# Optimization experiments

Hardware: AMD Instinct MI355X
Metric: run time of the kernel (lower is better)

## Reference

```python
import jax, jax.numpy as jnp
import numpy as np

IMG_H, IMG_W = 256, 704
STRIDE = 4.0


def _make_cams(B, Ncam):
    K = np.array([[560.0, 0.0, 352.0], [0.0, 560.0, 128.0], [0.0, 0.0, 1.0]], dtype=np.float32)
    intrinsics = np.broadcast_to(K, (B, Ncam, 3, 3)).copy()
    c2e = np.zeros((Ncam, 4, 4), dtype=np.float32)
    for i in range(Ncam):
        th = 2.0 * np.pi * i / Ncam
        x_cam = np.array([np.sin(th), -np.cos(th), 0.0])   # camera right in ego
        y_cam = np.array([0.0, 0.0, -1.0])                  # camera down in ego
        z_cam = np.array([np.cos(th), np.sin(th), 0.0])     # camera forward in ego
        c2e[i, :3, 0] = x_cam
        c2e[i, :3, 1] = y_cam
        c2e[i, :3, 2] = z_cam
        c2e[i, :3, 3] = np.array([0.0, 0.0, 1.5])           # camera mounted 1.5m up
        c2e[i, 3, 3] = 1.0
    cam2ego = np.broadcast_to(c2e, (B, Ncam, 4, 4)).copy()
    return jnp.asarray(intrinsics), jnp.asarray(cam2ego)


def setup_inputs() -> dict:
    key = jax.random.key(0)
    B, Npts, Ncam = 4, 500000, 6
    Hf, Wf = 64, 176
    k1, k2, k3 = jax.random.split(key, 3)
    xy = jax.random.uniform(k1, (B, Npts, 2), minval=-50.0, maxval=50.0, dtype=jnp.float32)
    z = jax.random.uniform(k2, (B, Npts, 1), minval=-5.0, maxval=3.0, dtype=jnp.float32)
    inten = jax.random.uniform(k3, (B, Npts, 1), dtype=jnp.float32)
    points_ego = jnp.concatenate([xy, z, inten], axis=-1)
    intrinsics, cam2ego = _make_cams(B, Ncam)
    # depth_values = linspace(1, 48, 48), step 1 -> edges [0.5, 1.5, ..., 48.5]
    dv = np.arange(48, dtype=np.float32) + 1.0
    step = 1.0
    edges = np.concatenate([[dv[0] - step / 2.0], dv + step / 2.0]).astype(np.float32)
    return {
        "points_ego": points_ego,
        "intrinsics": intrinsics,
        "cam2ego": cam2ego,
        "bin_edges": jnp.asarray(edges),
        "Hf": Hf,
        "Wf": Wf,
    }


def reference(points_ego, intrinsics, cam2ego, bin_edges, Hf, Wf):
    B, Npts, _ = points_ego.shape
    Ncam = intrinsics.shape[1]
    num_bins = bin_edges.shape[0] - 1

    ego2cam = jnp.linalg.inv(cam2ego)                       # (B,N,4,4)
    pts_h = jnp.concatenate([points_ego[..., :3], jnp.ones_like(points_ego[..., :1])], axis=-1)
    # project all points into all cameras at once: (B,N,P,4)
    p_cam = jnp.einsum('bnij,bpj->bnpi', ego2cam, pts_h)
    x, y, z = p_cam[..., 0], p_cam[..., 1], p_cam[..., 2]
    zc = jnp.maximum(z, 1e-6)

    fx = intrinsics[:, :, 0, 0][:, :, None]
    fy = intrinsics[:, :, 1, 1][:, :, None]
    cx = intrinsics[:, :, 0, 2][:, :, None]
    cy = intrinsics[:, :, 1, 2][:, :, None]
    u = fx * (x / zc) + cx
    v = fy * (y / zc) + cy

    valid = (z > 0.1) & (u >= 0) & (u <= IMG_W - 1) & (v >= 0) & (v <= IMG_H - 1)
    uf = jnp.floor(u / STRIDE).astype(jnp.int32)
    vf = jnp.floor(v / STRIDE).astype(jnp.int32)
    valid = valid & (uf >= 0) & (uf < Wf) & (vf >= 0) & (vf < Hf)
    uf = jnp.clip(uf, 0, Wf - 1)
    vf = jnp.clip(vf, 0, Hf - 1)

    pix = vf * Wf + uf                                      # (B,N,P)
    bn = (jnp.arange(B, dtype=jnp.int32)[:, None] * Ncam + jnp.arange(Ncam, dtype=jnp.int32)[None, :])
    seg = (bn[:, :, None] * (Hf * Wf) + pix).reshape(-1)    # global segment per (b, cam, pixel)

    # z-buffer: min depth per pixel (invalid points -> +inf, empty segments -> +inf)
    z_flat = jnp.where(valid, z, jnp.inf).reshape(-1)
    z_min = jax.ops.segment_min(z_flat, seg, num_segments=B * Ncam * Hf * Wf)

    d = jnp.clip(z_min, bin_edges[0] + 0.001, bin_edges[-1] - 0.001)
    # torch.bucketize(right=False): edges[i-1] < v <= edges[i]  ->  searchsorted side='left'
    bin_id = jnp.clip(jnp.searchsorted(bin_edges, d, side='left') - 1, 0, num_bins - 1)
    labels = jnp.where(jnp.isfinite(z_min), bin_id, -1).astype(jnp.int32)
    return labels.reshape(B, Ncam, Hf, Wf)
```

## Files before the change

kernel.cpp:

```cpp
#include <hip/hip_runtime.h>
#include <stdint.h>

#define BB    4
#define NCAM  6
#define HF    64
#define WF    176
#define IMGPIX (HF * WF)
#define NIMG  (BB * NCAM)
#define NPIX  (NIMG * IMGPIX)
#define NEDGE 49
#define SENTINEL 0x7F7F7F7F

#define GER_FMA     1
#define TRSM_RECIP  1
#define TRSM_FMA    1

__device__ void inv4_sgesv(const float* __restrict__ m,
                           const float* __restrict__ K,
                           float* __restrict__ out) {
#pragma clang fp contract(off)
    float a[4][4];
    for (int i = 0; i < 4; ++i)
        for (int j = 0; j < 4; ++j)
            a[i][j] = m[i * 4 + j];

    int ipiv[4];
    for (int j = 0; j < 4; ++j) {
        int p = j;
        float best = fabsf(a[j][j]);
        for (int i = j + 1; i < 4; ++i) {
            float v = fabsf(a[i][j]);
            if (v > best) { best = v; p = i; }
        }
        ipiv[j] = p;
        if (p != j) {
            for (int k = 0; k < 4; ++k) {
                float t = a[j][k]; a[j][k] = a[p][k]; a[p][k] = t;
            }
        }
        float r = 1.0f / a[j][j];
        for (int i = j + 1; i < 4; ++i) a[i][j] = a[i][j] * r;
        for (int k = j + 1; k < 4; ++k) {
            float temp = -a[j][k];
            for (int i = j + 1; i < 4; ++i) {
#if GER_FMA
                a[i][k] = __builtin_fmaf(a[i][j], temp, a[i][k]);
#else
                a[i][k] = a[i][k] + a[i][j] * temp;
#endif
            }
        }
    }

    float bmat[4][4];
    for (int i = 0; i < 4; ++i)
        for (int j = 0; j < 4; ++j)
            bmat[i][j] = (i == j) ? 1.0f : 0.0f;

    for (int k = 0; k < 4; ++k) {
        int p = ipiv[k];
        if (p != k) {
            for (int c = 0; c < 4; ++c) {
                float t = bmat[k][c]; bmat[k][c] = bmat[p][c]; bmat[p][c] = t;
            }
        }
    }

    for (int c = 0; c < 4; ++c) {
        for (int k = 0; k < 4; ++k) {
            float bk = bmat[k][c];
            for (int i = k + 1; i < 4; ++i) {
#if TRSM_FMA
                bmat[i][c] = __builtin_fmaf(a[i][k], -bk, bmat[i][c]);
#else
                bmat[i][c] = bmat[i][c] - a[i][k] * bk;
#endif
            }
        }
    }

#if TRSM_RECIP
    float rdiag[4];
    for (int k = 0; k < 4; ++k) rdiag[k] = 1.0f / a[k][k];
#endif
    for (int c = 0; c < 4; ++c) {
        for (int k = 3; k >= 0; --k) {
#if TRSM_RECIP
            bmat[k][c] = bmat[k][c] * rdiag[k];
#else
            bmat[k][c] = bmat[k][c] / a[k][k];
#endif
            float bk = bmat[k][c];
            for (int i = 0; i < k; ++i) {
#if TRSM_FMA
                bmat[i][c] = __builtin_fmaf(a[i][k], -bk, bmat[i][c]);
#else
                bmat[i][c] = bmat[i][c] - a[i][k] * bk;
#endif
            }
        }
    }

    for (int i = 0; i < 3; ++i)
        for (int j = 0; j < 4; ++j)
            out[i * 4 + j] = bmat[i][j];

    out[12] = K[0];
    out[13] = K[4];
    out[14] = K[2];
    out[15] = K[5];
}

__global__ void prep_cams_f32(const float* __restrict__ intr,
                              const float* __restrict__ c2e,
                              float* __restrict__ cams) {
    int idx = blockIdx.x * blockDim.x + threadIdx.x;
    if (idx >= NIMG) return;
    inv4_sgesv(c2e + idx * 16, intr + idx * 9, cams + idx * 16);
}

__device__ __forceinline__ bool project_pair(const float* M, float px, float py,
                                             float pz, float lo, float hi,
                                             int& pix, int& label) {
#pragma clang fp contract(off)
    float x = M[3];  x = x + M[2]  * pz;  x = x + M[1] * py;  x = x + M[0] * px;
    float y = M[7];  y = y + M[6]  * pz;  y = y + M[5] * py;  y = y + M[4] * px;
    float z = M[11]; z = z + M[10] * pz;  z = z + M[9] * py;  z = z + M[8] * px;

    float zc = fmaxf(z, 1e-6f);
    float u = M[12] * (x / zc) + M[14];
    float v = M[13] * (y / zc) + M[15];

    bool ok = (z > 0.1f) && (u >= 0.0f) && (u <= 703.0f) &&
              (v >= 0.0f) && (v <= 255.0f);

    int uf = (int)floorf(u / 4.0f);
    int vf = (int)floorf(v / 4.0f);
    pix = vf * WF + uf;

    float d = fminf(fmaxf(z, lo), hi);
    label = (int)ceilf(d - 0.5f) - 1;
    return ok;
}

__global__ __launch_bounds__(1024)
void scatter_lds(const float4* __restrict__ pts,
                 const float* __restrict__ cams,
                 const float* __restrict__ edges_f,
                 uint8_t* __restrict__ reps,
                 int npts, int csz) {
    __shared__ unsigned sbuf[IMGPIX];

    int g   = blockIdx.x;
    int img = blockIdx.y;
    int b   = img / NCAM;

    for (int i = threadIdx.x; i < IMGPIX; i += 1024)
        sbuf[i] = 0xFFFFFFFFu;
    __syncthreads();

    const float* M = cams + img * 16;
    float lo = edges_f[0]         + 0.001f;
    float hi = edges_f[NEDGE - 1] - 0.001f;

    int start = g * csz;
    int end   = start + csz; if (end > npts) end = npts;
    const float4* bp = pts + (size_t)b * npts;

    int p = start + (int)threadIdx.x;

    for (; p + 3 * 1024 < end; p += 4 * 1024) {
        float4 a0 = bp[p];
        float4 a1 = bp[p + 1024];
        float4 a2 = bp[p + 2048];
        float4 a3 = bp[p + 3072];

        int px0, l0, px1, l1, px2, l2, px3, l3;
        bool k0 = project_pair(M, a0.x, a0.y, a0.z, lo, hi, px0, l0);
        bool k1 = project_pair(M, a1.x, a1.y, a1.z, lo, hi, px1, l1);
        bool k2 = project_pair(M, a2.x, a2.y, a2.z, lo, hi, px2, l2);
        bool k3 = project_pair(M, a3.x, a3.y, a3.z, lo, hi, px3, l3);

        if (k0) atomicMin(&sbuf[px0], (unsigned)l0);
        if (k1) atomicMin(&sbuf[px1], (unsigned)l1);
        if (k2) atomicMin(&sbuf[px2], (unsigned)l2);
        if (k3) atomicMin(&sbuf[px3], (unsigned)l3);
    }
    for (; p < end; p += 1024) {
        float4 a0 = bp[p];
        int px0, l0;
        if (project_pair(M, a0.x, a0.y, a0.z, lo, hi, px0, l0))
            atomicMin(&sbuf[px0], (unsigned)l0);
    }
    __syncthreads();

    uint8_t* r = reps + (size_t)g * NPIX + (size_t)img * IMGPIX;
    for (int i = threadIdx.x; i < IMGPIX; i += 1024)
        r[i] = (uint8_t)sbuf[i];
}

__global__ void merge_reps(const uint8_t* __restrict__ reps, int G,
                           int* __restrict__ out) {
    int q = blockIdx.x * blockDim.x + threadIdx.x;
    if (q >= NPIX / 4) return;

    unsigned m = 0xFFFFFFFFu;
    for (int g = 0; g < G; ++g) {
        unsigned v = *(const unsigned*)(reps + (size_t)g * NPIX + q * 4);
        unsigned lo0 = (m & 0xFFu),        v0 = (v & 0xFFu);
        unsigned lo1 = (m >> 8) & 0xFFu,   v1 = (v >> 8) & 0xFFu;
        unsigned lo2 = (m >> 16) & 0xFFu,  v2 = (v >> 16) & 0xFFu;
        unsigned lo3 = (m >> 24),          v3 = (v >> 24);
        lo0 = v0 < lo0 ? v0 : lo0;
        lo1 = v1 < lo1 ? v1 : lo1;
        lo2 = v2 < lo2 ? v2 : lo2;
        lo3 = v3 < lo3 ? v3 : lo3;
        m = lo0 | (lo1 << 8) | (lo2 << 16) | (lo3 << 24);
    }
    int4 r;
    unsigned b0 = m & 0xFFu, b1 = (m >> 8) & 0xFFu,
             b2 = (m >> 16) & 0xFFu, b3 = m >> 24;
    r.x = (b0 == 255u) ? -1 : (int)b0;
    r.y = (b1 == 255u) ? -1 : (int)b1;
    r.z = (b2 == 255u) ? -1 : (int)b2;
    r.w = (b3 == 255u) ? -1 : (int)b3;
    ((int4*)out)[q] = r;
}

__global__ __launch_bounds__(256)
void scatter_minbin(const float4* __restrict__ pts,
                    const float* __restrict__ cams,
                    const float* __restrict__ edges_f,
                    int* __restrict__ out,
                    int npts) {
    int p = blockIdx.x * blockDim.x + threadIdx.x;
    int b = blockIdx.y;
    if (p >= npts) return;

    float4 pt = pts[(size_t)b * npts + p];
    float lo = edges_f[0]         + 0.001f;
    float hi = edges_f[NEDGE - 1] - 0.001f;

#pragma unroll
    for (int n = 0; n < NCAM; ++n) {
        const float* M = cams + (b * NCAM + n) * 16;
        int pix, label;
        if (project_pair(M, pt.x, pt.y, pt.z, lo, hi, pix, label)) {
            atomicMin(&out[(b * NCAM + n) * IMGPIX + pix], label);
        }
    }
}

__global__ void finalize(int* out) {
    int i = blockIdx.x * blockDim.x + threadIdx.x;
    if (i < NPIX && out[i] == SENTINEL) out[i] = -1;
}

extern "C" void kernel_launch(void* const* d_in, const int* in_sizes, int n_in,
                              void* d_out, int out_size, void* d_ws, size_t ws_size,
                              hipStream_t stream) {
    const float* points    = (const float*)d_in[0];
    const float* intrinsic = (const float*)d_in[1];
    const float* cam2ego   = (const float*)d_in[2];
    const float* edges     = (const float*)d_in[3];

    int npts = in_sizes[0] / (BB * 4);
    int* out = (int*)d_out;

    float*   cams = (float*)d_ws;
    uint8_t* reps = (uint8_t*)d_ws + 2048;

    int G = 0;
    if (ws_size > 2048 + (size_t)NPIX)
        G = (int)((ws_size - 2048) / (size_t)NPIX);
    if (G > 21) G = 21;

    prep_cams_f32<<<1, 64, 0, stream>>>(intrinsic, cam2ego, cams);

    if (G >= 1) {
        int csz = (npts + G - 1) / G;
        dim3 grid(G, NIMG);
        scatter_lds<<<grid, 1024, 0, stream>>>((const float4*)points, cams,
                                               edges, reps, npts, csz);
        merge_reps<<<(NPIX / 4 + 255) / 256, 256, 0, stream>>>(reps, G, out);
    } else {
        hipMemsetAsync(out, 0x7F, (size_t)NPIX * sizeof(int), stream);
        dim3 grid((npts + 255) / 256, BB);
        scatter_minbin<<<grid, 256, 0, stream>>>((const float4*)points, cams,
                                                 edges, out, npts);
        finalize<<<(NPIX + 255) / 256, 256, 0, stream>>>(out);
    }
}
```

Before: 48.83 us.

## Project each point into three cameras per block to reuse point loads

Each block now keeps three camera z-buffers in LDS (about 135 KB) and projects every loaded point into all three cameras, so point data is read from global memory once per three cameras instead of once per camera. The grid shrinks to 8 camera groups, and G rises to 30 to recover parallelism. The floor is replaced by a truncating cast on a multiply, which is only safe because negative u and v are already masked. The LDS init is vectorised and the output is packed into 32-bit stores. Occupancy drops to one block per CU because of the larger LDS footprint.

```diff
diff --git a/kernel.cpp b/kernel.cpp
--- a/kernel.cpp
+++ b/kernel.cpp
@@ -134,8 +134,8 @@
     bool ok = (z > 0.1f) && (u >= 0.0f) && (u <= 703.0f) &&
               (v >= 0.0f) && (v <= 255.0f);
 
-    int uf = (int)floorf(u / 4.0f);
-    int vf = (int)floorf(v / 4.0f);
+    int uf = (int)(u * 0.25f);
+    int vf = (int)(v * 0.25f);
     pix = vf * WF + uf;
 
     float d = fminf(fmaxf(z, lo), hi);
@@ -144,22 +144,26 @@
 }
 
 __global__ __launch_bounds__(1024)
-void scatter_lds(const float4* __restrict__ pts,
-                 const float* __restrict__ cams,
-                 const float* __restrict__ edges_f,
-                 uint8_t* __restrict__ reps,
-                 int npts, int csz) {
-    __shared__ unsigned sbuf[IMGPIX];
-
-    int g   = blockIdx.x;
-    int img = blockIdx.y;
-    int b   = img / NCAM;
-
-    for (int i = threadIdx.x; i < IMGPIX; i += 1024)
-        sbuf[i] = 0xFFFFFFFFu;
+void scatter_lds3(const float4* __restrict__ pts,
+                  const float* __restrict__ cams,
+                  const float* __restrict__ edges_f,
+                  uint8_t* __restrict__ reps,
+                  int npts, int csz) {
+    __shared__ unsigned sbuf[3 * IMGPIX];
+
+    int g    = blockIdx.x;
+    int grp  = blockIdx.y;
+    int img0 = grp * 3;
+    int b    = grp >> 1;
+
+    uint4* s4 = (uint4*)sbuf;
+    for (int i = threadIdx.x; i < 3 * IMGPIX / 4; i += 1024)
+        s4[i] = make_uint4(0xFFFFFFFFu, 0xFFFFFFFFu, 0xFFFFFFFFu, 0xFFFFFFFFu);
     __syncthreads();
 
-    const float* M = cams + img * 16;
+    const float* M0 = cams + (img0 + 0) * 16;
+    const float* M1 = cams + (img0 + 1) * 16;
+    const float* M2 = cams + (img0 + 2) * 16;
     float lo = edges_f[0]         + 0.001f;
     float hi = edges_f[NEDGE - 1] - 0.001f;
 
@@ -169,34 +173,49 @@
 
     int p = start + (int)threadIdx.x;
 
-    for (; p + 3 * 1024 < end; p += 4 * 1024) {
+    for (; p + 1024 < end; p += 2 * 1024) {
         float4 a0 = bp[p];
         float4 a1 = bp[p + 1024];
-        float4 a2 = bp[p + 2048];
-        float4 a3 = bp[p + 3072];
-
-        int px0, l0, px1, l1, px2, l2, px3, l3;
-        bool k0 = project_pair(M, a0.x, a0.y, a0.z, lo, hi, px0, l0);
-        bool k1 = project_pair(M, a1.x, a1.y, a1.z, lo, hi, px1, l1);
-        bool k2 = project_pair(M, a2.x, a2.y, a2.z, lo, hi, px2, l2);
-        bool k3 = project_pair(M, a3.x, a3.y, a3.z, lo, hi, px3, l3);
-
-        if (k0) atomicMin(&sbuf[px0], (unsigned)l0);
-        if (k1) atomicMin(&sbuf[px1], (unsigned)l1);
-        if (k2) atomicMin(&sbuf[px2], (unsigned)l2);
-        if (k3) atomicMin(&sbuf[px3], (unsigned)l3);
+
+        int x00, l00, x01, l01, x10, l10, x11, l11, x20, l20, x21, l21;
+        bool k00 = project_pair(M0, a0.x, a0.y, a0.z, lo, hi, x00, l00);
+        bool k01 = project_pair(M0, a1.x, a1.y, a1.z, lo, hi, x01, l01);
+        bool k10 = project_pair(M1, a0.x, a0.y, a0.z, lo, hi, x10, l10);
+        bool k11 = project_pair(M1, a1.x, a1.y, a1.z, lo, hi, x11, l11);
+        bool k20 = project_pair(M2, a0.x, a0.y, a0.z, lo, hi, x20, l20);
+        bool k21 = project_pair(M2, a1.x, a1.y, a1.z, lo, hi, x21, l21);
+
+        if (k00) atomicMin(&sbuf[x00],              (unsigned)l00);
+        if (k01) atomicMin(&sbuf[x01],              (unsigned)l01);
+        if (k10) atomicMin(&sbuf[IMGPIX + x10],     (unsigned)l10);
+        if (k11) atomicMin(&sbuf[IMGPIX + x11],     (unsigned)l11);
+        if (k20) atomicMin(&sbuf[2 * IMGPIX + x20], (unsigned)l20);
+        if (k21) atomicMin(&sbuf[2 * IMGPIX + x21], (unsigned)l21);
     }
     for (; p < end; p += 1024) {
         float4 a0 = bp[p];
-        int px0, l0;
-        if (project_pair(M, a0.x, a0.y, a0.z, lo, hi, px0, l0))
-            atomicMin(&sbuf[px0], (unsigned)l0);
+        int x0, l0, x1, l1, x2, l2;
+        if (project_pair(M0, a0.x, a0.y, a0.z, lo, hi, x0, l0))
+            atomicMin(&sbuf[x0], (unsigned)l0);
+        if (project_pair(M1, a0.x, a0.y, a0.z, lo, hi, x1, l1))
+            atomicMin(&sbuf[IMGPIX + x1], (unsigned)l1);
+        if (project_pair(M2, a0.x, a0.y, a0.z, lo, hi, x2, l2))
+            atomicMin(&sbuf[2 * IMGPIX + x2], (unsigned)l2);
     }
     __syncthreads();
 
-    uint8_t* r = reps + (size_t)g * NPIX + (size_t)img * IMGPIX;
-    for (int i = threadIdx.x; i < IMGPIX; i += 1024)
-        r[i] = (uint8_t)sbuf[i];
+    for (int c = 0; c < 3; ++c) {
+        unsigned* r32 = (unsigned*)(reps + (size_t)g * NPIX +
+                                    (size_t)(img0 + c) * IMGPIX);
+        const unsigned* s = &sbuf[c * IMGPIX];
+        for (int i = threadIdx.x; i < IMGPIX / 4; i += 1024) {
+            unsigned w = (s[4 * i] & 0xFFu)
+                       | ((s[4 * i + 1] & 0xFFu) << 8)
+                       | ((s[4 * i + 2] & 0xFFu) << 16)
+                       | ((s[4 * i + 3] & 0xFFu) << 24);
+            r32[i] = w;
+        }
+    }
 }
 
 __global__ void merge_reps(const uint8_t* __restrict__ reps, int G,
@@ -273,15 +292,15 @@
     int G = 0;
     if (ws_size > 2048 + (size_t)NPIX)
         G = (int)((ws_size - 2048) / (size_t)NPIX);
-    if (G > 21) G = 21;
+    if (G > 30) G = 30;
 
     prep_cams_f32<<<1, 64, 0, stream>>>(intrinsic, cam2ego, cams);
 
     if (G >= 1) {
         int csz = (npts + G - 1) / G;
-        dim3 grid(G, NIMG);
-        scatter_lds<<<grid, 1024, 0, stream>>>((const float4*)points, cams,
-                                               edges, reps, npts, csz);
+        dim3 grid(G, NIMG / 3);
+        scatter_lds3<<<grid, 1024, 0, stream>>>((const float4*)points, cams,
+                                                edges, reps, npts, csz);
         merge_reps<<<(NPIX / 4 + 255) / 256, 256, 0, stream>>>(reps, G, out);
     } else {
         hipMemsetAsync(out, 0x7F, (size_t)NPIX * sizeof(int), stream);
```

Result: faster. 46.52 us (-4.7%).
